# Performance work log

Measured on AMD Instinct MI355X. Metric: run time of the kernel, lower is better.

## Reference

```python
import jax, jax.numpy as jnp
import numpy as np

EPS = 1e-5

def _act_quant(x):
    # per-token int8 absmax quantization (BitNet b1.58)
    scale = 127.0 / jnp.clip(jnp.max(jnp.abs(x), axis=-1, keepdims=True), EPS)
    return jnp.clip(jnp.round(x * scale), -128.0, 127.0) / scale

def _weight_quant(w):
    # per-tensor ternary quantization: round(w/mean|w|) clipped to {-1,0,1}
    scale = 1.0 / jnp.clip(jnp.mean(jnp.abs(w)), EPS)
    return jnp.clip(jnp.round(w * scale), -1.0, 1.0) / scale

def _ste(x, q):
    # straight-through estimator: forward uses q, backward passes through x
    return x + jax.lax.stop_gradient(q - x)

def bitlinear(x, w):
    xq = _ste(x, _act_quant(x))
    wq = _ste(w, _weight_quant(w))
    return jnp.einsum('btd,hd->bth', xq, wq)

def setup_inputs() -> dict:
    key = jax.random.key(0)
    k1, k2, k3 = jax.random.split(key, 3)
    B, T, D, H = 4, 1024, 2048, 8192
    x = jax.random.normal(k1, (B, T, D), dtype=jnp.float32)
    w1 = jax.random.normal(k2, (H, D), dtype=jnp.float32) * 0.02
    w2 = jax.random.normal(k3, (D, H), dtype=jnp.float32) * 0.02
    return {"x": x, "w1": w1, "w2": w2}

def reference(x, w1, w2):
    h = jax.nn.relu(bitlinear(x, w1))   # [B, T, H]
    out = bitlinear(h, w2)              # [B, T, D]
    return out
```

## Files before the change

kernel.cpp:

```cpp
#include <hip/hip_runtime.h>
#include <hip/hip_bf16.h>

#define EPSF 1e-5f

typedef int v4i __attribute__((ext_vector_type(4)));
typedef short v8s __attribute__((ext_vector_type(8)));

static constexpr int BB = 4, TT = 1024, DD = 2048, HH = 8192;
static constexpr int MROWS = BB * TT;
static constexpr long long WCOUNT = (long long)DD * HH;


__device__ __forceinline__ void async_copy16(const void* g, void* l) {
  __builtin_amdgcn_global_load_lds(
      (const __attribute__((address_space(1))) unsigned int*)g,
      (__attribute__((address_space(3))) unsigned int*)l,
      16, 0, 0);
}

__device__ __forceinline__ int pack4(float a, float b, float c, float d,
                                     float scale, float lo, float hi) {
  int ia = (int)fminf(fmaxf(rintf(a * scale), lo), hi);
  int ib = (int)fminf(fmaxf(rintf(b * scale), lo), hi);
  int ic = (int)fminf(fmaxf(rintf(c * scale), lo), hi);
  int id = (int)fminf(fmaxf(rintf(d * scale), lo), hi);
  return (ia & 0xff) | ((ib & 0xff) << 8) | ((ic & 0xff) << 16) | ((id & 0xff) << 24);
}

__device__ __forceinline__ float blockMaxF256(float v) {
  #pragma unroll
  for (int off = 32; off; off >>= 1) v = fmaxf(v, __shfl_down(v, off, 64));
  __shared__ float sm[4];
  int lane = threadIdx.x & 63, wv = threadIdx.x >> 6;
  if (lane == 0) sm[wv] = v;
  __syncthreads();
  return fmaxf(fmaxf(sm[0], sm[1]), fmaxf(sm[2], sm[3]));
}

__device__ __forceinline__ int blockMaxI256(int v) {
  #pragma unroll
  for (int off = 32; off; off >>= 1) v = max(v, __shfl_down(v, off, 64));
  __shared__ int sm[4];
  int lane = threadIdx.x & 63, wv = threadIdx.x >> 6;
  if (lane == 0) sm[wv] = v;
  __syncthreads();
  return max(max(sm[0], sm[1]), max(sm[2], sm[3]));
}

__device__ __forceinline__ void swizzle_tiles(int& mt, int& nt) {
  int Mt = gridDim.y, Nt = gridDim.x;
  int id = blockIdx.y * Nt + blockIdx.x;
  int c = id & 7, k = id >> 3;
  int pm = (Mt >= Nt) ? 4 : 2;
  int PM = Mt / pm, PN = Nt / (8 / pm);
  int pr = c % pm, pc = c / pm;
  mt = pr * PM + (k % PM);
  nt = pc * PN + (k / PM);
}


__global__ __launch_bounds__(256) void abs_sum_kernel(
    const float* __restrict__ w1, const float* __restrict__ w2,
    double* __restrict__ sums) {
  const float* w = blockIdx.y ? w2 : w1;
  const float4* w4 = (const float4*)w;
  long long n4 = WCOUNT / 4;
  float s = 0.f;
  for (long long i = (long long)blockIdx.x * blockDim.x + threadIdx.x; i < n4;
       i += (long long)gridDim.x * blockDim.x) {
    float4 v = w4[i];
    s += fabsf(v.x) + fabsf(v.y) + fabsf(v.z) + fabsf(v.w);
  }
  #pragma unroll
  for (int off = 32; off; off >>= 1) s += __shfl_down(s, off, 64);
  __shared__ float sm[4];
  int lane = threadIdx.x & 63, wv = threadIdx.x >> 6;
  if (lane == 0) sm[wv] = s;
  __syncthreads();
  if (threadIdx.x == 0) {
    float t = sm[0] + sm[1] + sm[2] + sm[3];
    atomicAdd(&sums[blockIdx.y], (double)t);
  }
}


__global__ __launch_bounds__(256) void quant_w_kernel(
    const float* __restrict__ w1, const float* __restrict__ w2,
    const double* __restrict__ sums,
    signed char* __restrict__ q1, signed char* __restrict__ q2) {
  const float* w = blockIdx.y ? w2 : w1;
  signed char* q = blockIdx.y ? q2 : q1;
  float mean = fmaxf((float)(sums[blockIdx.y] * (1.0 / (double)WCOUNT)), EPSF);
  float scale = 1.0f / mean;
  const float4* w4 = (const float4*)w;
  int* q4 = (int*)q;
  long long n4 = WCOUNT / 4;
  for (long long i = (long long)blockIdx.x * blockDim.x + threadIdx.x; i < n4;
       i += (long long)gridDim.x * blockDim.x) {
    float4 v = w4[i];
    q4[i] = pack4(v.x, v.y, v.z, v.w, scale, -1.f, 1.f);
  }
}


__global__ __launch_bounds__(256) void quant_x_kernel(
    const float* __restrict__ x, signed char* __restrict__ xq,
    float* __restrict__ ascale) {
  int row = blockIdx.x;
  const float4* xr = (const float4*)(x + (size_t)row * DD);
  int t = threadIdx.x;
  float4 v0 = xr[2 * t], v1 = xr[2 * t + 1];
  float m = fmaxf(fmaxf(fabsf(v0.x), fabsf(v0.y)), fmaxf(fabsf(v0.z), fabsf(v0.w)));
  m = fmaxf(m, fmaxf(fmaxf(fabsf(v1.x), fabsf(v1.y)), fmaxf(fabsf(v1.z), fabsf(v1.w))));
  float am = fmaxf(blockMaxF256(m), EPSF);
  float scale = 127.0f / am;
  int* out = (int*)(xq + (size_t)row * DD);
  out[2 * t]     = pack4(v0.x, v0.y, v0.z, v0.w, scale, -128.f, 127.f);
  out[2 * t + 1] = pack4(v1.x, v1.y, v1.z, v1.w, scale, -128.f, 127.f);
  if (t == 0) ascale[row] = am / 127.0f;
}


__global__ __launch_bounds__(256) void quant_h_kernel(
    const short* __restrict__ h, signed char* __restrict__ hq,
    float* __restrict__ a2, const float* __restrict__ a1,
    const double* __restrict__ sums) {
  int row = blockIdx.x;
  int t = threadIdx.x;
  const v8s* hr = (const v8s*)(h + (size_t)row * HH);
  v8s v[4];
  int mx = 0;
  #pragma unroll
  for (int i = 0; i < 4; i++) {
    v[i] = hr[t + i * 256];
    #pragma unroll
    for (int j = 0; j < 8; j++) mx = max(mx, (int)v[i][j]);
  }
  int bmx = blockMaxI256(mx);
  float wmean1 = fmaxf((float)(sums[0] * (1.0 / (double)WCOUNT)), EPSF);
  float f = a1[row] * wmean1;
  float maxh = (float)bmx * f;
  float am = fmaxf(maxh, EPSF);
  float scale = 127.0f / am;
  int* out = (int*)(hq + (size_t)row * HH);
  #pragma unroll
  for (int i = 0; i < 4; i++) {
    out[(t + i * 256) * 2] =
        pack4((float)v[i][0] * f, (float)v[i][1] * f, (float)v[i][2] * f,
              (float)v[i][3] * f, scale, -128.f, 127.f);
    out[(t + i * 256) * 2 + 1] =
        pack4((float)v[i][4] * f, (float)v[i][5] * f, (float)v[i][6] * f,
              (float)v[i][7] * f, scale, -128.f, 127.f);
  }
  if (t == 0) a2[row] = am / 127.0f;
}


template <int MODE, int BK>
__global__ __launch_bounds__(256) void gemm_i8_kernel(
    const signed char* __restrict__ A, const signed char* __restrict__ B,
    void* __restrict__ Cout, const float* __restrict__ ascale,
    const double* __restrict__ wsum, int M, int N, int K) {
  constexpr int CH = BK / 16;
  constexpr int SEGROWS = 1024 / BK;
  constexpr int SPW = BK / 32;
  __shared__ signed char As[128 * BK];
  __shared__ signed char Bs[128 * BK];

  const int t = threadIdx.x;
  const int lane = t & 63, wv = t >> 6;
  const int wm = wv >> 1, wn = wv & 1;
  int mt, nt;
  swizzle_tiles(mt, nt);
  const int m0 = mt * 128, n0 = nt * 128;
  const int q = lane >> 4;

  const signed char* aSrc[SPW];
  const signed char* bSrc[SPW];
  #pragma unroll
  for (int i = 0; i < SPW; i++) {
    int seg = wv * SPW + i;
    int r = seg * SEGROWS + lane / CH;
    int c = (lane % CH) ^ (r & (CH - 1));
    aSrc[i] = A + (size_t)(m0 + r) * K + c * 16;
    bSrc[i] = B + (size_t)(n0 + r) * K + c * 16;
  }

  v4i acc[4][4];
  #pragma unroll
  for (int i = 0; i < 4; i++)
    #pragma unroll
    for (int j = 0; j < 4; j++) {
      v4i z = {0, 0, 0, 0};
      acc[i][j] = z;
    }

  int rowA[4], rowB[4];
  #pragma unroll
  for (int i = 0; i < 4; i++) {
    rowA[i] = wm * 64 + i * 16 + (lane & 15);
    rowB[i] = wn * 64 + i * 16 + (lane & 15);
  }

  for (int k0 = 0; k0 < K; k0 += BK) {
    #pragma unroll
    for (int i = 0; i < SPW; i++) {
      async_copy16(aSrc[i] + k0, &As[(wv * SPW + i) * 1024]);
      async_copy16(bSrc[i] + k0, &Bs[(wv * SPW + i) * 1024]);
    }
    __syncthreads();
    #pragma unroll
    for (int kc = 0; kc < CH / 4; kc++) {
      v4i af[4], bf[4];
      #pragma unroll
      for (int i = 0; i < 4; i++) {
        int ca = (kc * 4 + q) ^ (rowA[i] & (CH - 1));
        af[i] = *(const v4i*)(As + rowA[i] * BK + ca * 16);
        int cb = (kc * 4 + q) ^ (rowB[i] & (CH - 1));
        bf[i] = *(const v4i*)(Bs + rowB[i] * BK + cb * 16);
      }
      #pragma unroll
      for (int i = 0; i < 4; i++)
        #pragma unroll
        for (int j = 0; j < 4; j++)
          acc[i][j] = __builtin_amdgcn_mfma_i32_16x16x64_i8(af[i], bf[j], acc[i][j], 0, 0, 0);
    }
    __syncthreads();
  }

  if constexpr (MODE == 1) {
    short* C = (short*)Cout;
    #pragma unroll
    for (int i = 0; i < 4; i++) {
      int mBase = m0 + wm * 64 + i * 16 + q * 4;
      #pragma unroll
      for (int e = 0; e < 4; e++) {
        #pragma unroll
        for (int j = 0; j < 4; j++) {
          int n = n0 + wn * 64 + j * 16 + (lane & 15);
          int r = acc[i][j][e];
          r = r < 0 ? 0 : (r > 32767 ? 32767 : r);
          C[(size_t)(mBase + e) * N + n] = (short)r;
        }
      }
    }
  } else {
    float* C = (float*)Cout;
    float wmean = fmaxf((float)(wsum[0] * (1.0 / (double)WCOUNT)), EPSF);
    #pragma unroll
    for (int i = 0; i < 4; i++) {
      int mBase = m0 + wm * 64 + i * 16 + q * 4;
      #pragma unroll
      for (int e = 0; e < 4; e++) {
        float f = ascale[mBase + e] * wmean;
        #pragma unroll
        for (int j = 0; j < 4; j++) {
          int n = n0 + wn * 64 + j * 16 + (lane & 15);
          C[(size_t)(mBase + e) * N + n] = (float)acc[i][j][e] * f;
        }
      }
    }
  }
}


extern "C" void kernel_launch(void* const* d_in, const int* in_sizes, int n_in,
                              void* d_out, int out_size, void* d_ws, size_t ws_size,
                              hipStream_t stream) {
  const float* x  = (const float*)d_in[0];
  const float* w1 = (const float*)d_in[1];
  const float* w2 = (const float*)d_in[2];
  float* out = (float*)d_out;

  char* ws = (char*)d_ws;
  double* sums = (double*)ws;
  float* a1 = (float*)(ws + 256);
  float* a2 = (float*)(ws + 256 + 16384);
  signed char* w1q = (signed char*)(ws + 33024);
  signed char* w2q = w1q + (size_t)WCOUNT;
  signed char* xq  = w2q + (size_t)WCOUNT;
  signed char* hq  = xq + (size_t)MROWS * DD;
  short* h16 = (short*)(hq + (size_t)MROWS * HH);

  hipMemsetAsync(sums, 0, 16, stream);
  abs_sum_kernel<<<dim3(1024, 2), 256, 0, stream>>>(w1, w2, sums);
  quant_w_kernel<<<dim3(2048, 2), 256, 0, stream>>>(w1, w2, sums, w1q, w2q);
  quant_x_kernel<<<MROWS, 256, 0, stream>>>(x, xq, a1);
  gemm_i8_kernel<1, 128><<<dim3(HH / 128, MROWS / 128), 256, 0, stream>>>(
      xq, w1q, h16, nullptr, nullptr, MROWS, HH, DD);
  quant_h_kernel<<<MROWS, 256, 0, stream>>>(h16, hq, a2, a1, sums);
  gemm_i8_kernel<0, 256><<<dim3(DD / 128, MROWS / 128), 256, 0, stream>>>(
      hq, w2q, out, a2, &sums[1], MROWS, DD, HH);
}
```

Baseline: 389.9 us.

## Load B fragments directly from global into registers, drop B LDS staging

The int8 GEMM no longer stages the weight (B) tile in shared memory. Each wave instead loads its own B fragments from global memory straight into registers and prefetches the next k-chunk one step ahead. The A tile still goes through LDS with BK fixed at 256. The second GEMM now uses 64-wide N tiles with 128 threads, which halves LDS use per block and allows more blocks per CU. The trade-off is redundant global loads of B across waves and exposed global latency inside the MFMA loop.

```diff
diff --git a/kernel.cpp b/kernel.cpp
--- a/kernel.cpp
+++ b/kernel.cpp
@@ -156,34 +156,39 @@
 }
 
 
-template <int MODE, int BK>
-__global__ __launch_bounds__(256) void gemm_i8_kernel(
+template <int MODE, int WNW>
+__global__ __launch_bounds__(128 * WNW) void gemm_i8_kernel(
     const signed char* __restrict__ A, const signed char* __restrict__ B,
     void* __restrict__ Cout, const float* __restrict__ ascale,
     const double* __restrict__ wsum, int M, int N, int K) {
+  constexpr int BK = 256;
   constexpr int CH = BK / 16;
-  constexpr int SEGROWS = 1024 / BK;
-  constexpr int SPW = BK / 32;
+  constexpr int WAVES = 2 * WNW;
+  constexpr int SPW = 16 / WNW;
   __shared__ signed char As[128 * BK];
-  __shared__ signed char Bs[128 * BK];
 
   const int t = threadIdx.x;
   const int lane = t & 63, wv = t >> 6;
-  const int wm = wv >> 1, wn = wv & 1;
+  const int wm = wv / WNW, wn = wv % WNW;
   int mt, nt;
   swizzle_tiles(mt, nt);
-  const int m0 = mt * 128, n0 = nt * 128;
+  const int m0 = mt * 128, n0 = nt * (64 * WNW);
   const int q = lane >> 4;
 
   const signed char* aSrc[SPW];
-  const signed char* bSrc[SPW];
   #pragma unroll
   for (int i = 0; i < SPW; i++) {
     int seg = wv * SPW + i;
-    int r = seg * SEGROWS + lane / CH;
-    int c = (lane % CH) ^ (r & (CH - 1));
+    int r = seg * 4 + (lane >> 4);
+    int c = (lane & 15) ^ (r & 15);
     aSrc[i] = A + (size_t)(m0 + r) * K + c * 16;
-    bSrc[i] = B + (size_t)(n0 + r) * K + c * 16;
+  }
+
+  const signed char* bPtr[4];
+  #pragma unroll
+  for (int j = 0; j < 4; j++) {
+    int row = n0 + wn * 64 + j * 16 + (lane & 15);
+    bPtr[j] = B + (size_t)row * K + q * 16;
   }
 
   v4i acc[4][4];
@@ -195,35 +200,38 @@
       acc[i][j] = z;
     }
 
-  int rowA[4], rowB[4];
-  #pragma unroll
-  for (int i = 0; i < 4; i++) {
-    rowA[i] = wm * 64 + i * 16 + (lane & 15);
-    rowB[i] = wn * 64 + i * 16 + (lane & 15);
-  }
+  int rowA[4];
+  #pragma unroll
+  for (int i = 0; i < 4; i++) rowA[i] = wm * 64 + i * 16 + (lane & 15);
 
   for (int k0 = 0; k0 < K; k0 += BK) {
     #pragma unroll
-    for (int i = 0; i < SPW; i++) {
+    for (int i = 0; i < SPW; i++)
       async_copy16(aSrc[i] + k0, &As[(wv * SPW + i) * 1024]);
-      async_copy16(bSrc[i] + k0, &Bs[(wv * SPW + i) * 1024]);
-    }
+    v4i bcur[4], bnxt[4];
+    #pragma unroll
+    for (int j = 0; j < 4; j++) bcur[j] = *(const v4i*)(bPtr[j] + k0);
     __syncthreads();
     #pragma unroll
-    for (int kc = 0; kc < CH / 4; kc++) {
-      v4i af[4], bf[4];
+    for (int kc = 0; kc < 4; kc++) {
+      if (kc < 3) {
+        #pragma unroll
+        for (int j = 0; j < 4; j++)
+          bnxt[j] = *(const v4i*)(bPtr[j] + k0 + (kc + 1) * 64);
+      }
+      v4i af[4];
       #pragma unroll
       for (int i = 0; i < 4; i++) {
-        int ca = (kc * 4 + q) ^ (rowA[i] & (CH - 1));
+        int ca = (kc * 4 + q) ^ (rowA[i] & 15);
         af[i] = *(const v4i*)(As + rowA[i] * BK + ca * 16);
-        int cb = (kc * 4 + q) ^ (rowB[i] & (CH - 1));
-        bf[i] = *(const v4i*)(Bs + rowB[i] * BK + cb * 16);
       }
       #pragma unroll
       for (int i = 0; i < 4; i++)
         #pragma unroll
         for (int j = 0; j < 4; j++)
-          acc[i][j] = __builtin_amdgcn_mfma_i32_16x16x64_i8(af[i], bf[j], acc[i][j], 0, 0, 0);
+          acc[i][j] = __builtin_amdgcn_mfma_i32_16x16x64_i8(af[i], bcur[j], acc[i][j], 0, 0, 0);
+      #pragma unroll
+      for (int j = 0; j < 4; j++) bcur[j] = bnxt[j];
     }
     __syncthreads();
   }
@@ -286,9 +294,9 @@
   abs_sum_kernel<<<dim3(1024, 2), 256, 0, stream>>>(w1, w2, sums);
   quant_w_kernel<<<dim3(2048, 2), 256, 0, stream>>>(w1, w2, sums, w1q, w2q);
   quant_x_kernel<<<MROWS, 256, 0, stream>>>(x, xq, a1);
-  gemm_i8_kernel<1, 128><<<dim3(HH / 128, MROWS / 128), 256, 0, stream>>>(
+  gemm_i8_kernel<1, 2><<<dim3(HH / 128, MROWS / 128), 256, 0, stream>>>(
       xq, w1q, h16, nullptr, nullptr, MROWS, HH, DD);
   quant_h_kernel<<<MROWS, 256, 0, stream>>>(h16, hq, a2, a1, sums);
-  gemm_i8_kernel<0, 256><<<dim3(DD / 128, MROWS / 128), 256, 0, stream>>>(
+  gemm_i8_kernel<0, 1><<<dim3(DD / 64, MROWS / 128), 128, 0, stream>>>(
       hq, w2q, out, a2, &sums[1], MROWS, DD, HH);
 }
```

Result: slower. 538.2 us (+38.0%).

## Fuse weight abs-sum, weight quant and activation quant into one cooperative kernel

Applied to the files above, without the earlier changes.

Replaces the memset, abs-sum, weight-quant and x-quant launches with one cooperative-launch kernel. Blocks write per-block partial sums, quantize x rows, then after a grid-wide sync reduce the partials and ternarize both weights in the same kernel. The scalar weight means are precomputed once as floats for the later kernels. This removes launch gaps and the global double atomics, at the cost of a grid barrier and of needing all 1024 blocks co-resident; the old four-kernel path is kept as a fallback if the cooperative launch fails.

```diff
diff --git a/kernel.cpp b/kernel.cpp
--- a/kernel.cpp
+++ b/kernel.cpp
@@ -1,5 +1,8 @@
 #include <hip/hip_runtime.h>
 #include <hip/hip_bf16.h>
+#include <hip/hip_cooperative_groups.h>
+
+namespace cg = cooperative_groups;
 
 #define EPSF 1e-5f
 
@@ -25,16 +28,6 @@
   int ic = (int)fminf(fmaxf(rintf(c * scale), lo), hi);
   int id = (int)fminf(fmaxf(rintf(d * scale), lo), hi);
   return (ia & 0xff) | ((ib & 0xff) << 8) | ((ic & 0xff) << 16) | ((id & 0xff) << 24);
-}
-
-__device__ __forceinline__ float blockMaxF256(float v) {
-  #pragma unroll
-  for (int off = 32; off; off >>= 1) v = fmaxf(v, __shfl_down(v, off, 64));
-  __shared__ float sm[4];
-  int lane = threadIdx.x & 63, wv = threadIdx.x >> 6;
-  if (lane == 0) sm[wv] = v;
-  __syncthreads();
-  return fmaxf(fmaxf(sm[0], sm[1]), fmaxf(sm[2], sm[3]));
 }
 
 __device__ __forceinline__ int blockMaxI256(int v) {
@@ -56,6 +49,90 @@
   int pr = c % pm, pc = c / pm;
   mt = pr * PM + (k % PM);
   nt = pc * PN + (k / PM);
+}
+
+
+__global__ __launch_bounds__(256, 4) void fused_pre_kernel(
+    const float* __restrict__ w1, const float* __restrict__ w2,
+    const float* __restrict__ x, float* __restrict__ meanw,
+    float* __restrict__ partials, signed char* __restrict__ w1q,
+    signed char* __restrict__ w2q, signed char* __restrict__ xq,
+    float* __restrict__ a1) {
+  const int t = threadIdx.x, bid = blockIdx.x;
+  const int lane = t & 63, wv = t >> 6;
+  const long long n4 = WCOUNT / 4;
+  const long long stride = (long long)gridDim.x * blockDim.x;
+  const float4* w14 = (const float4*)w1;
+  const float4* w24 = (const float4*)w2;
+
+  float s1 = 0.f, s2 = 0.f;
+  for (long long i = (long long)bid * blockDim.x + t; i < n4; i += stride) {
+    float4 u = w14[i], v = w24[i];
+    s1 += fabsf(u.x) + fabsf(u.y) + fabsf(u.z) + fabsf(u.w);
+    s2 += fabsf(v.x) + fabsf(v.y) + fabsf(v.z) + fabsf(v.w);
+  }
+  #pragma unroll
+  for (int off = 32; off; off >>= 1) {
+    s1 += __shfl_down(s1, off, 64);
+    s2 += __shfl_down(s2, off, 64);
+  }
+  __shared__ float sms[8];
+  if (lane == 0) { sms[wv] = s1; sms[wv + 4] = s2; }
+  __syncthreads();
+  if (t == 0) {
+    partials[bid] = sms[0] + sms[1] + sms[2] + sms[3];
+    partials[1024 + bid] = sms[4] + sms[5] + sms[6] + sms[7];
+  }
+
+  __shared__ float smx[4];
+  #pragma unroll
+  for (int r = 0; r < 4; r++) {
+    int row = bid * 4 + r;
+    const float4* xr = (const float4*)(x + (size_t)row * DD);
+    float4 v0 = xr[2 * t], v1 = xr[2 * t + 1];
+    float m = fmaxf(fmaxf(fabsf(v0.x), fabsf(v0.y)), fmaxf(fabsf(v0.z), fabsf(v0.w)));
+    m = fmaxf(m, fmaxf(fmaxf(fabsf(v1.x), fabsf(v1.y)), fmaxf(fabsf(v1.z), fabsf(v1.w))));
+    #pragma unroll
+    for (int off = 32; off; off >>= 1) m = fmaxf(m, __shfl_down(m, off, 64));
+    if (lane == 0) smx[wv] = m;
+    __syncthreads();
+    float am = fmaxf(fmaxf(fmaxf(smx[0], smx[1]), fmaxf(smx[2], smx[3])), EPSF);
+    float scale = 127.0f / am;
+    int* outp = (int*)(xq + (size_t)row * DD);
+    outp[2 * t]     = pack4(v0.x, v0.y, v0.z, v0.w, scale, -128.f, 127.f);
+    outp[2 * t + 1] = pack4(v1.x, v1.y, v1.z, v1.w, scale, -128.f, 127.f);
+    if (t == 0) a1[row] = am / 127.0f;
+    __syncthreads();
+  }
+
+  cg::this_grid().sync();
+
+  double d1 = (double)partials[t] + (double)partials[t + 256] +
+              (double)partials[t + 512] + (double)partials[t + 768];
+  double d2 = (double)partials[1024 + t] + (double)partials[1280 + t] +
+              (double)partials[1536 + t] + (double)partials[1792 + t];
+  #pragma unroll
+  for (int off = 32; off; off >>= 1) {
+    d1 += __shfl_down(d1, off, 64);
+    d2 += __shfl_down(d2, off, 64);
+  }
+  __shared__ double smd[8];
+  if (lane == 0) { smd[wv] = d1; smd[wv + 4] = d2; }
+  __syncthreads();
+  double sum1 = smd[0] + smd[1] + smd[2] + smd[3];
+  double sum2 = smd[4] + smd[5] + smd[6] + smd[7];
+  float mean1 = fmaxf((float)(sum1 * (1.0 / (double)WCOUNT)), EPSF);
+  float mean2 = fmaxf((float)(sum2 * (1.0 / (double)WCOUNT)), EPSF);
+  if (bid == 0 && t == 0) { meanw[0] = mean1; meanw[1] = mean2; }
+
+  float sc1 = 1.0f / mean1, sc2 = 1.0f / mean2;
+  int* q14 = (int*)w1q;
+  int* q24 = (int*)w2q;
+  for (long long i = (long long)bid * blockDim.x + t; i < n4; i += stride) {
+    float4 u = w14[i], v = w24[i];
+    q14[i] = pack4(u.x, u.y, u.z, u.w, sc1, -1.f, 1.f);
+    q24[i] = pack4(v.x, v.y, v.z, v.w, sc2, -1.f, 1.f);
+  }
 }
 
 
@@ -77,20 +154,18 @@
   int lane = threadIdx.x & 63, wv = threadIdx.x >> 6;
   if (lane == 0) sm[wv] = s;
   __syncthreads();
-  if (threadIdx.x == 0) {
-    float t = sm[0] + sm[1] + sm[2] + sm[3];
-    atomicAdd(&sums[blockIdx.y], (double)t);
-  }
-}
-
+  if (threadIdx.x == 0)
+    atomicAdd(&sums[blockIdx.y], (double)(sm[0] + sm[1] + sm[2] + sm[3]));
+}
 
 __global__ __launch_bounds__(256) void quant_w_kernel(
     const float* __restrict__ w1, const float* __restrict__ w2,
-    const double* __restrict__ sums,
+    const double* __restrict__ sums, float* __restrict__ meanw,
     signed char* __restrict__ q1, signed char* __restrict__ q2) {
   const float* w = blockIdx.y ? w2 : w1;
   signed char* q = blockIdx.y ? q2 : q1;
   float mean = fmaxf((float)(sums[blockIdx.y] * (1.0 / (double)WCOUNT)), EPSF);
+  if (blockIdx.x == 0 && threadIdx.x == 0) meanw[blockIdx.y] = mean;
   float scale = 1.0f / mean;
   const float4* w4 = (const float4*)w;
   int* q4 = (int*)q;
@@ -102,17 +177,22 @@
   }
 }
 
-
 __global__ __launch_bounds__(256) void quant_x_kernel(
     const float* __restrict__ x, signed char* __restrict__ xq,
     float* __restrict__ ascale) {
   int row = blockIdx.x;
   const float4* xr = (const float4*)(x + (size_t)row * DD);
   int t = threadIdx.x;
+  int lane = t & 63, wv = t >> 6;
   float4 v0 = xr[2 * t], v1 = xr[2 * t + 1];
   float m = fmaxf(fmaxf(fabsf(v0.x), fabsf(v0.y)), fmaxf(fabsf(v0.z), fabsf(v0.w)));
   m = fmaxf(m, fmaxf(fmaxf(fabsf(v1.x), fabsf(v1.y)), fmaxf(fabsf(v1.z), fabsf(v1.w))));
-  float am = fmaxf(blockMaxF256(m), EPSF);
+  #pragma unroll
+  for (int off = 32; off; off >>= 1) m = fmaxf(m, __shfl_down(m, off, 64));
+  __shared__ float sm[4];
+  if (lane == 0) sm[wv] = m;
+  __syncthreads();
+  float am = fmaxf(fmaxf(fmaxf(sm[0], sm[1]), fmaxf(sm[2], sm[3])), EPSF);
   float scale = 127.0f / am;
   int* out = (int*)(xq + (size_t)row * DD);
   out[2 * t]     = pack4(v0.x, v0.y, v0.z, v0.w, scale, -128.f, 127.f);
@@ -124,7 +204,7 @@
 __global__ __launch_bounds__(256) void quant_h_kernel(
     const short* __restrict__ h, signed char* __restrict__ hq,
     float* __restrict__ a2, const float* __restrict__ a1,
-    const double* __restrict__ sums) {
+    const float* __restrict__ meanw) {
   int row = blockIdx.x;
   int t = threadIdx.x;
   const v8s* hr = (const v8s*)(h + (size_t)row * HH);
@@ -137,8 +217,7 @@
     for (int j = 0; j < 8; j++) mx = max(mx, (int)v[i][j]);
   }
   int bmx = blockMaxI256(mx);
-  float wmean1 = fmaxf((float)(sums[0] * (1.0 / (double)WCOUNT)), EPSF);
-  float f = a1[row] * wmean1;
+  float f = a1[row] * meanw[0];
   float maxh = (float)bmx * f;
   float am = fmaxf(maxh, EPSF);
   float scale = 127.0f / am;
@@ -160,7 +239,7 @@
 __global__ __launch_bounds__(256) void gemm_i8_kernel(
     const signed char* __restrict__ A, const signed char* __restrict__ B,
     void* __restrict__ Cout, const float* __restrict__ ascale,
-    const double* __restrict__ wsum, int M, int N, int K) {
+    const float* __restrict__ wmean_p, int M, int N, int K) {
   constexpr int CH = BK / 16;
   constexpr int SEGROWS = 1024 / BK;
   constexpr int SPW = BK / 32;
@@ -246,7 +325,7 @@
     }
   } else {
     float* C = (float*)Cout;
-    float wmean = fmaxf((float)(wsum[0] * (1.0 / (double)WCOUNT)), EPSF);
+    float wmean = wmean_p[0];
     #pragma unroll
     for (int i = 0; i < 4; i++) {
       int mBase = m0 + wm * 64 + i * 16 + q * 4;
@@ -273,22 +352,35 @@
   float* out = (float*)d_out;
 
   char* ws = (char*)d_ws;
-  double* sums = (double*)ws;
-  float* a1 = (float*)(ws + 256);
-  float* a2 = (float*)(ws + 256 + 16384);
-  signed char* w1q = (signed char*)(ws + 33024);
+  float* meanw = (float*)ws;
+  double* sums = (double*)(ws + 128);
+  float* partials = (float*)(ws + 256);
+  float* a1 = (float*)(ws + 16384);
+  float* a2 = (float*)(ws + 32768);
+  signed char* w1q = (signed char*)(ws + 65536);
   signed char* w2q = w1q + (size_t)WCOUNT;
   signed char* xq  = w2q + (size_t)WCOUNT;
   signed char* hq  = xq + (size_t)MROWS * DD;
   short* h16 = (short*)(hq + (size_t)MROWS * HH);
 
-  hipMemsetAsync(sums, 0, 16, stream);
-  abs_sum_kernel<<<dim3(1024, 2), 256, 0, stream>>>(w1, w2, sums);
-  quant_w_kernel<<<dim3(2048, 2), 256, 0, stream>>>(w1, w2, sums, w1q, w2q);
-  quant_x_kernel<<<MROWS, 256, 0, stream>>>(x, xq, a1);
+  {
+    const float* aw1 = w1; const float* aw2 = w2; const float* ax = x;
+    float* ameanw = meanw; float* apart = partials;
+    signed char* aq1 = w1q; signed char* aq2 = w2q; signed char* axq = xq;
+    float* aa1 = a1;
+    void* args[] = {&aw1, &aw2, &ax, &ameanw, &apart, &aq1, &aq2, &axq, &aa1};
+    hipError_t ce = hipLaunchCooperativeKernel(
+        (const void*)fused_pre_kernel, dim3(1024), dim3(256), args, 0, stream);
+    if (ce != hipSuccess) {
+      hipMemsetAsync(sums, 0, 16, stream);
+      abs_sum_kernel<<<dim3(1024, 2), 256, 0, stream>>>(w1, w2, sums);
+      quant_w_kernel<<<dim3(2048, 2), 256, 0, stream>>>(w1, w2, sums, meanw, w1q, w2q);
+      quant_x_kernel<<<MROWS, 256, 0, stream>>>(x, xq, a1);
+    }
+  }
   gemm_i8_kernel<1, 128><<<dim3(HH / 128, MROWS / 128), 256, 0, stream>>>(
-      xq, w1q, h16, nullptr, nullptr, MROWS, HH, DD);
-  quant_h_kernel<<<MROWS, 256, 0, stream>>>(h16, hq, a2, a1, sums);
+      xq, w1q, h16, nullptr, meanw, MROWS, HH, DD);
+  quant_h_kernel<<<MROWS, 256, 0, stream>>>(h16, hq, a2, a1, meanw);
   gemm_i8_kernel<0, 256><<<dim3(DD / 128, MROWS / 128), 256, 0, stream>>>(
-      hq, w2q, out, a2, &sums[1], MROWS, DD, HH);
-}
+      hq, w2q, out, a2, &meanw[1], MROWS, DD, HH);
+}
```

Result: slower. 475.7 us (+22.0%).
